# Optimization experiments

Hardware: AMD Instinct MI355X
Metric: run time of the kernel (lower is better)

Reference implementation:

```python
import jax, jax.numpy as jnp
import numpy as np

# ---- layer config (yolov3, layer_no=2) ----
STRIDE = 8
N_CLASSES = 80
IGNORE_TH = 0.7
ANCHORS_PX = np.array([[10,13],[16,30],[33,23],[30,61],[62,45],[59,119],[116,90],[156,198],[373,326]], np.float32)
ALL_ANCHORS = ANCHORS_PX / STRIDE          # [9,2] in grid units
ANCHOR_ID_LO, ANCHOR_ID_HI = 0, 2          # anchor_mask[2] = [0,1,2]
ANCHORS = ALL_ANCHORS[ANCHOR_ID_LO:ANCHOR_ID_HI+1]  # [3,2]
NA = 3
NC = N_CLASSES + 5

B, IN_CH, NG, NBOX = 16, 256, 76, 50


def _safe_log(p):
    # emulate torch BCE's log clamp at -100; eps stops 0*inf -> nan
    return jnp.maximum(jnp.log(jnp.maximum(p, 1e-12)), -100.0)


def _bce_sum(p, t, w=None):
    l = -(t * _safe_log(p) + (1.0 - t) * _safe_log(1.0 - p))
    if w is not None:
        l = l * w
    return l.sum()


def setup_inputs() -> dict:
    key = jax.random.key(0)
    k1, k2, k3, k4, k5 = jax.random.split(key, 5)
    xin = jax.random.normal(k1, (B, IN_CH, NG, NG), jnp.float32)
    cls = jax.random.randint(k2, (B, NBOX, 1), 0, N_CLASSES).astype(jnp.float32)
    cxy = jax.random.uniform(k3, (B, NBOX, 2), jnp.float32, 0.02, 0.98)
    wh = jax.random.uniform(k4, (B, NBOX, 2), jnp.float32, 0.02, 0.40)
    labels = jnp.concatenate([cls, cxy, wh], axis=-1)  # [B,N,5]
    W = jax.random.normal(k5, (NA * NC, IN_CH), jnp.float32) * 0.02  # 1x1 conv
    b = jnp.zeros((NA * NC,), jnp.float32)
    return {"xin": xin, "labels": labels, "W": W, "b": b}


def _yolo_loss(xin, labels, W, b):
    nB, _, nG, _ = xin.shape
    anchors = jnp.asarray(ANCHORS, xin.dtype)          # [3,2]
    all_anchors = jnp.asarray(ALL_ANCHORS, xin.dtype)  # [9,2]

    # 1x1 conv -> [B, A, G, G, C]
    x = jnp.einsum('bchw,oc->bohw', xin, W) + b[None, :, None, None]
    x = x.reshape(nB, NA, NC, nG, nG).transpose(0, 1, 3, 4, 2)

    xy = jax.nn.sigmoid(x[..., :2])
    wh = x[..., 2:4]
    conf_cls = jax.nn.sigmoid(x[..., 4:])  # [B,A,G,G,1+ncls]

    gy, gx = jnp.meshgrid(jnp.arange(nG, dtype=x.dtype), jnp.arange(nG, dtype=x.dtype), indexing='ij')
    pred_boxes = jnp.stack([
        xy[..., 0] + gx,
        xy[..., 1] + gy,
        jnp.exp(wh[..., 0]) * anchors[:, 0][None, :, None, None],
        jnp.exp(wh[..., 1]) * anchors[:, 1][None, :, None, None]], axis=-1)  # [B,A,G,G,4]

    # ---- ground truth ----
    valid = labels.sum(-1) > 0                     # [B,N]
    gt_cls = labels[..., 0].astype(jnp.int32)
    gt = labels[..., 1:] * nG                      # [B,N,4] cx,cy,w,h in grid units
    gt_x, gt_y, gt_w, gt_h = gt[..., 0], gt[..., 1], gt[..., 2], gt[..., 3]
    gi = jnp.floor(gt_x).astype(jnp.int32)
    gj = jnp.floor(gt_y).astype(jnp.int32)

    # best anchor per gt: wh-IoU vs all 9 anchors (centered at origin)
    inter_a = jnp.minimum(gt_w[..., None], all_anchors[:, 0]) * jnp.minimum(gt_h[..., None], all_anchors[:, 1])
    union_a = gt_w[..., None] * gt_h[..., None] + all_anchors[:, 0] * all_anchors[:, 1] - inter_a
    best = jnp.argmax(inter_a / union_a, axis=-1)  # [B,N]
    in_mask = (best >= ANCHOR_ID_LO) & (best <= ANCHOR_ID_HI)
    a = jnp.where(in_mask, best % 3, -1)           # [B,N]

    # all-pairs IoU: pred boxes vs gt boxes (ignore mask)
    pb = pred_boxes.reshape(nB, -1, 4)             # [B,M,4], M = A*G*G
    pa_area = pb[..., 2] * pb[..., 3]
    gt_area = gt_w * gt_h
    tl = jnp.maximum(pb[:, :, None, :2] - pb[:, :, None, 2:] / 2, gt[:, None, :, :2] - gt[:, None, :, 2:] / 2)
    br = jnp.minimum(pb[:, :, None, :2] + pb[:, :, None, 2:] / 2, gt[:, None, :, :2] + gt[:, None, :, 2:] / 2)
    inter = jnp.prod(br - tl, -1) * jnp.all(tl < br, -1)
    iou = inter / (pa_area[:, :, None] + gt_area[:, None, :] - inter)
    iou = jnp.where(valid[:, None, :], iou, 0.0)
    best_iou = iou.max(-1)                         # [B,M]
    has_boxes = valid.any(-1)
    obj_mask = jnp.where(has_boxes[:, None], best_iou <= IGNORE_TH, True).reshape(nB, NA, nG, nG)

    # ---- scatter target assignment ----
    assign = valid & (a >= 0)
    a_safe = jnp.clip(a, 0, NA - 1)
    aw = anchors[a_safe, 0]
    ah = anchors[a_safe, 1]
    tvec = jnp.concatenate([
        (gt_x - jnp.floor(gt_x))[..., None],
        (gt_y - jnp.floor(gt_y))[..., None],
        jnp.log(gt_w / aw + 1e-16)[..., None],
        jnp.log(gt_h / ah + 1e-16)[..., None],
        jnp.ones_like(gt_x)[..., None],
        jax.nn.one_hot(gt_cls, N_CLASSES, dtype=x.dtype)], axis=-1)  # [B,N,NC]
    sval = 2.0 - gt_w * gt_h / (nG * nG)

    bf = jnp.broadcast_to(jnp.arange(nB)[:, None], a.shape).reshape(-1)
    af = jnp.where(assign, a_safe, NA).reshape(-1)  # NA is OOB -> dropped
    jf = gj.reshape(-1)
    if_ = gi.reshape(-1)

    target = jnp.zeros((nB, NA, nG, nG, NC), x.dtype).at[bf, af, jf, if_].set(tvec.reshape(-1, NC), mode='drop')
    scale = jnp.zeros((nB, NA, nG, nG), x.dtype).at[bf, af, jf, if_].set(sval.reshape(-1), mode='drop')
    obj_mask = obj_mask.at[bf, af, jf, if_].set(True, mode='drop')
    noobj = jnp.zeros((nB, NA, nG, nG), bool).at[bf, af, jf, if_].set(True, mode='drop')

    # ---- losses ----
    nm = noobj.astype(x.dtype)[..., None]
    p_obj = conf_cls[..., 0] * obj_mask
    t_obj = target[..., 4] * obj_mask
    p_xy = xy * nm
    t_xy = target[..., :2] * nm
    p_wh = wh * nm
    t_wh = target[..., 2:4] * nm
    p_cls = conf_cls[..., 1:] * nm
    t_cls = target[..., 5:] * nm
    sc = scale[..., None]

    loss_xy = _bce_sum(p_xy, t_xy, sc)
    rs = jnp.sqrt(sc)
    loss_wh = 0.5 * jnp.sum((p_wh * rs - t_wh * rs) ** 2)
    loss_obj = _bce_sum(p_obj, t_obj)
    loss_cls = _bce_sum(p_cls, t_cls)
    loss = loss_xy + loss_wh + loss_obj + loss_cls
    return jnp.stack([loss, loss_xy, loss_wh, loss_obj, loss_cls])


def reference(xin, labels, W, b):
    return _yolo_loss(xin, labels, W, b)
```

## Files before the change

kernel.cpp:

```cpp
#include <hip/hip_runtime.h>
#include <math.h>

#define NB    16
#define NAg   3
#define NCg   85
#define NCLS  80
#define NGg   76
#define NSp   (NGg*NGg)
#define NBOX  50
#define INCH  256

#define ACC_OFF  0
#define HAS_OFF  32
#define WT_OFF   128
#define GB_OFF   (WT_OFF + 16384)
#define GA_OFF   (GB_OFF + 25600)
#define GI_OFF   (GA_OFF + 25600)
#define ZERO_BYTES 96

__device__ __constant__ float c_AW[9] = {1.25f,2.0f,4.125f,3.75f,7.75f,7.375f,14.5f,19.5f,46.625f};
__device__ __constant__ float c_AH[9] = {1.625f,3.75f,2.875f,7.625f,5.625f,14.875f,11.25f,24.75f,40.75f};

__device__ __forceinline__ float safe_log(float p) {
    return fmaxf(logf(fmaxf(p, 1e-12f)), -100.0f);
}
__device__ __forceinline__ float sigm(float x) {
    return 1.0f / (1.0f + expf(-x));
}

__global__ __launch_bounds__(256) void k_labels(
    const float* __restrict__ labels, const float* __restrict__ W,
    float* __restrict__ Wt, float* __restrict__ gbox, float* __restrict__ gaux,
    int* __restrict__ gint, int* __restrict__ hasAny)
{
    const int t = blockIdx.x * 256 + threadIdx.x;

    if (t < INCH * 16) {
        const int c = t >> 4, f = t & 15;
        Wt[t] = (f < 15) ? W[((f / 5) * NCg + (f % 5)) * INCH + c] : 0.f;
    }
    if (t >= NB * NBOX) return;
    const int b = t / NBOX;

    const float* L = labels + (size_t)t * 5;
    const float l0 = L[0], l1 = L[1], l2 = L[2], l3 = L[3], l4 = L[4];
    const int valid = (l0 + l1 + l2 + l3 + l4) > 0.f;

    const float gx = l1 * NGg, gy = l2 * NGg, gw = l3 * NGg, gh = l4 * NGg;

    int best = 0; float brr = -1.f;
#pragma unroll
    for (int k = 0; k < 9; k++) {
        float inter = fminf(gw, c_AW[k]) * fminf(gh, c_AH[k]);
        float uni   = gw*gh + c_AW[k]*c_AH[k] - inter;
        float r     = inter / uni;
        if (r > brr) { brr = r; best = k; }
    }
    const int a = (best <= 2) ? best : -1;
    const int assign = valid && (a >= 0);
    const int a_safe = a < 0 ? 0 : (a > 2 ? 2 : a);

    const int gi = (int)floorf(gx), gj = (int)floorf(gy);
    const int inb = (gi >= 0) && (gi < NGg) && (gj >= 0) && (gj < NGg);
    const int cell = (assign && inb) ? (a * NSp + gj * NGg + gi) : -1;

    float* gb = gbox + (size_t)t * 8;
    gb[0] = gx - gw * 0.5f;
    gb[1] = gy - gh * 0.5f;
    gb[2] = gx + gw * 0.5f;
    gb[3] = gy + gh * 0.5f;
    gb[4] = valid ? gw * gh : -1.f;
    gb[5] = __int_as_float(cell);

    float* ga = gaux + (size_t)t * 8;
    ga[0] = gx - floorf(gx);
    ga[1] = gy - floorf(gy);
    ga[2] = logf(gw / c_AW[a_safe] + 1e-16f);
    ga[3] = logf(gh / c_AH[a_safe] + 1e-16f);
    ga[4] = 2.f - gw * gh / (float)NSp;

    gint[t*2 + 0] = cell;
    gint[t*2 + 1] = (int)l0;

    if (valid) atomicOr(&hasAny[b], 1);
}

__global__ __launch_bounds__(64) void k_main(
    const float* __restrict__ xin, const float* __restrict__ Wt,
    const float* __restrict__ bias, const float* __restrict__ gbox,
    const int* __restrict__ hasAny, float* __restrict__ acc)
{
    const int b = blockIdx.y;
    const int s = blockIdx.x * 64 + threadIdx.x;

    float l = 0.f;
    if (s < NSp) {
        float accv[15];
#pragma unroll
        for (int f = 0; f < 15; ++f) accv[f] = 0.f;

        const float* xp = xin + (size_t)b * INCH * NSp + s;
#pragma unroll 2
        for (int c0 = 0; c0 < INCH; c0 += 8) {
            float v[8];
#pragma unroll
            for (int k = 0; k < 8; ++k) v[k] = xp[(size_t)(c0 + k) * NSp];
#pragma unroll
            for (int k = 0; k < 8; ++k) {
                const float* wr = Wt + ((c0 + k) << 4);
#pragma unroll
                for (int f = 0; f < 15; ++f) accv[f] += wr[f] * v[k];
            }
        }

        const int sy = s / NGg;
        const int sx = s - sy * NGg;
        const float gxf = (float)sx, gyf = (float)sy;

        float pbx0[3], pby0[3], pbx1[3], pby1[3], pa[3], cf[3];
#pragma unroll
        for (int a = 0; a < 3; ++a) {
            const float px = sigm(accv[a*5+0] + bias[a*NCg+0]) + gxf;
            const float py = sigm(accv[a*5+1] + bias[a*NCg+1]) + gyf;
            const float pw = expf(accv[a*5+2] + bias[a*NCg+2]) * c_AW[a];
            const float ph = expf(accv[a*5+3] + bias[a*NCg+3]) * c_AH[a];
            cf[a]  = sigm(accv[a*5+4] + bias[a*NCg+4]);
            pbx0[a] = px - pw * 0.5f;  pby0[a] = py - ph * 0.5f;
            pbx1[a] = px + pw * 0.5f;  pby1[a] = py + ph * 0.5f;
            pa[a]   = pw * ph;
        }

        bool ex0 = false, ex1 = false, ex2 = false;
        bool as0 = false, as1 = false, as2 = false;
        const float* gb = gbox + (size_t)b * NBOX * 8;
        for (int n = 0; n < NBOX; ++n) {
            const float bx0 = gb[n*8+0], by0 = gb[n*8+1];
            const float bx1 = gb[n*8+2], by1 = gb[n*8+3];
            const float gar = gb[n*8+4];
            const int cell  = __float_as_int(gb[n*8+5]);
            const int d = cell - s;
            as0 = as0 || (d == 0);
            as1 = as1 || (d == NSp);
            as2 = as2 || (d == 2*NSp);
            if (gar >= 0.f) {
#pragma unroll
                for (int a = 0; a < 3; ++a) {
                    const float tlx = fmaxf(pbx0[a], bx0);
                    const float tly = fmaxf(pby0[a], by0);
                    const float brx = fminf(pbx1[a], bx1);
                    const float bry = fminf(pby1[a], by1);
                    const float dx = brx - tlx, dy = bry - tly;
                    const float inter = (dx > 0.f && dy > 0.f) ? dx * dy : 0.f;
                    const bool hit = inter > 0.7f * (pa[a] + gar - inter);
                    if      (a == 0) ex0 = ex0 || hit;
                    else if (a == 1) ex1 = ex1 || hit;
                    else             ex2 = ex2 || hit;
                }
            }
        }

        const bool hasB = hasAny[b] != 0;
#pragma unroll
        for (int a = 0; a < 3; ++a) {
            const bool ex = (a == 0) ? ex0 : ((a == 1) ? ex1 : ex2);
            const bool as = (a == 0) ? as0 : ((a == 1) ? as1 : as2);
            const bool maskpre = hasB ? (!ex) : true;
            if (maskpre || as) {
                const float c = cf[a];
                l += as ? -safe_log(c) : -safe_log(1.f - c);
            }
        }
    }

#pragma unroll
    for (int off = 32; off > 0; off >>= 1) l += __shfl_down(l, off);
    if (threadIdx.x == 0) atomicAdd(&acc[2], l);
}

__global__ __launch_bounds__(256) void k_assigned(
    const float* __restrict__ xin, const float* __restrict__ W,
    const float* __restrict__ bias, const float* __restrict__ gaux,
    const int* __restrict__ gint, float* __restrict__ acc)
{
    const int t = blockIdx.x;
    const int b = t / NBOX, n = t % NBOX;
    const int cell = gint[t*2];
    if (cell < 0) return;
    for (int n2 = n + 1; n2 < NBOX; ++n2)
        if (gint[(b*NBOX + n2)*2] == cell) return;

    const int a = cell / NSp, s = cell % NSp;
    const int o0 = a * NCg;
    const int tid = threadIdx.x;

    __shared__ float4 col4[64];
    __shared__ float  xsh[NCg];
    __shared__ float  sacc[3];

    ((float*)col4)[tid] = xin[((size_t)b * INCH + tid) * NSp + s];
    if (tid < 3) sacc[tid] = 0.f;
    __syncthreads();

    const int wid = tid >> 6, lane = tid & 63;
    for (int o = wid; o < NCg; o += 4) {
        const float4 wv = *(const float4*)&W[(size_t)(o0 + o) * INCH + lane * 4];
        const float4 cv = col4[lane];
        float p = wv.x*cv.x + wv.y*cv.y + wv.z*cv.z + wv.w*cv.w;
        for (int off = 32; off; off >>= 1) p += __shfl_down(p, off);
        if (lane == 0) xsh[o] = p + bias[o0 + o];
    }
    __syncthreads();

    if (tid < NCg) {
        const float* ga = gaux + (size_t)t * 8;
        const float sval = ga[4];
        const int gcls = gint[t*2 + 1];
        float val = xsh[tid];
        float term; int slot;
        if (tid < 2) {
            float tgt = ga[tid];
            float p = sigm(val);
            term = -(tgt * safe_log(p) + (1.f - tgt) * safe_log(1.f - p)) * sval;
            slot = 0;
        } else if (tid < 4) {
            float tgt = ga[tid];
            float d = val - tgt;
            term = 0.5f * sval * d * d;
            slot = 1;
        } else if (tid == 4) {
            term = 0.f; slot = 2;
        } else {
            float tgt = ((tid - 5) == gcls) ? 1.f : 0.f;
            float p = sigm(val);
            term = -(tgt * safe_log(p) + (1.f - tgt) * safe_log(1.f - p));
            slot = 2;
        }
        atomicAdd(&sacc[slot], term);
    }
    __syncthreads();
    if (tid == 0) {
        atomicAdd(&acc[0], sacc[0]);
        atomicAdd(&acc[1], sacc[1]);
        atomicAdd(&acc[3], sacc[2]);
    }
}

__global__ void k_final(const float* __restrict__ acc, float* __restrict__ out)
{
    float xy = acc[0], wh = acc[1], ob = acc[2], cl = acc[3];
    out[0] = xy + wh + ob + cl;
    out[1] = xy; out[2] = wh; out[3] = ob; out[4] = cl;
}

extern "C" void kernel_launch(void* const* d_in, const int* in_sizes, int n_in,
                              void* d_out, int out_size, void* d_ws, size_t ws_size,
                              hipStream_t stream)
{
    const float* xin    = (const float*)d_in[0];
    const float* labels = (const float*)d_in[1];
    const float* W      = (const float*)d_in[2];
    const float* bias   = (const float*)d_in[3];

    char* ws = (char*)d_ws;
    float* acc    = (float*)(ws + ACC_OFF);
    int*   hasAny = (int*)  (ws + HAS_OFF);
    float* Wt     = (float*)(ws + WT_OFF);
    float* gbox   = (float*)(ws + GB_OFF);
    float* gaux   = (float*)(ws + GA_OFF);
    int*   gint   = (int*)  (ws + GI_OFF);
    float* out    = (float*)d_out;

    hipMemsetAsync(ws, 0, ZERO_BYTES, stream);

    k_labels<<<16, 256, 0, stream>>>(labels, W, Wt, gbox, gaux, gint, hasAny);

    k_main<<<dim3((NSp + 63) / 64, NB), 64, 0, stream>>>(xin, Wt, bias, gbox, hasAny, acc);

    k_assigned<<<dim3(NB * NBOX), 256, 0, stream>>>(xin, W, bias, gaux, gint, acc);

    k_final<<<1, 1, 0, stream>>>(acc, out);
}
```

Measured before the change: 236.1 us.

## Split channel reduction and box loop across four waves per block in main kernel

The main kernel moves from 64-thread blocks to 256-thread blocks. Each of the four waves reduces a quarter of the input channels for the same 64 spatial positions, and the partial sums are combined through shared memory. The ground-truth box IoU loop is also split across the waves, with the results merged through OR-ed bitmasks in shared memory. The memset is folded into the labels kernel, which now assigns one block per batch and computes hasAny with a ballot instead of atomics. This raises parallelism and memory-level concurrency on the bandwidth-bound 1x1 conv, at the cost of extra shared-memory traffic and barriers.

Result: no change. 231.7 us (-1.9%).

```diff
diff --git a/kernel.cpp b/kernel.cpp
--- a/kernel.cpp
+++ b/kernel.cpp
@@ -16,7 +16,6 @@
 #define GB_OFF   (WT_OFF + 16384)
 #define GA_OFF   (GB_OFF + 25600)
 #define GI_OFF   (GA_OFF + 25600)
-#define ZERO_BYTES 96
 
 __device__ __constant__ float c_AW[9] = {1.25f,2.0f,4.125f,3.75f,7.75f,7.375f,14.5f,19.5f,46.625f};
 __device__ __constant__ float c_AH[9] = {1.625f,3.75f,2.875f,7.625f,5.625f,14.875f,11.25f,24.75f,40.75f};
@@ -31,117 +30,146 @@
 __global__ __launch_bounds__(256) void k_labels(
     const float* __restrict__ labels, const float* __restrict__ W,
     float* __restrict__ Wt, float* __restrict__ gbox, float* __restrict__ gaux,
-    int* __restrict__ gint, int* __restrict__ hasAny)
-{
-    const int t = blockIdx.x * 256 + threadIdx.x;
-
-    if (t < INCH * 16) {
+    int* __restrict__ gint, int* __restrict__ hasAny, float* __restrict__ acc)
+{
+    const int b = blockIdx.x, tid = threadIdx.x;
+    const int t = b * 256 + tid;
+
+    {
         const int c = t >> 4, f = t & 15;
         Wt[t] = (f < 15) ? W[((f / 5) * NCg + (f % 5)) * INCH + c] : 0.f;
     }
-    if (t >= NB * NBOX) return;
-    const int b = t / NBOX;
-
-    const float* L = labels + (size_t)t * 5;
-    const float l0 = L[0], l1 = L[1], l2 = L[2], l3 = L[3], l4 = L[4];
-    const int valid = (l0 + l1 + l2 + l3 + l4) > 0.f;
-
-    const float gx = l1 * NGg, gy = l2 * NGg, gw = l3 * NGg, gh = l4 * NGg;
-
-    int best = 0; float brr = -1.f;
-#pragma unroll
-    for (int k = 0; k < 9; k++) {
-        float inter = fminf(gw, c_AW[k]) * fminf(gh, c_AH[k]);
-        float uni   = gw*gh + c_AW[k]*c_AH[k] - inter;
-        float r     = inter / uni;
-        if (r > brr) { brr = r; best = k; }
-    }
-    const int a = (best <= 2) ? best : -1;
-    const int assign = valid && (a >= 0);
-    const int a_safe = a < 0 ? 0 : (a > 2 ? 2 : a);
-
-    const int gi = (int)floorf(gx), gj = (int)floorf(gy);
-    const int inb = (gi >= 0) && (gi < NGg) && (gj >= 0) && (gj < NGg);
-    const int cell = (assign && inb) ? (a * NSp + gj * NGg + gi) : -1;
-
-    float* gb = gbox + (size_t)t * 8;
-    gb[0] = gx - gw * 0.5f;
-    gb[1] = gy - gh * 0.5f;
-    gb[2] = gx + gw * 0.5f;
-    gb[3] = gy + gh * 0.5f;
-    gb[4] = valid ? gw * gh : -1.f;
-    gb[5] = __int_as_float(cell);
-
-    float* ga = gaux + (size_t)t * 8;
-    ga[0] = gx - floorf(gx);
-    ga[1] = gy - floorf(gy);
-    ga[2] = logf(gw / c_AW[a_safe] + 1e-16f);
-    ga[3] = logf(gh / c_AH[a_safe] + 1e-16f);
-    ga[4] = 2.f - gw * gh / (float)NSp;
-
-    gint[t*2 + 0] = cell;
-    gint[t*2 + 1] = (int)l0;
-
-    if (valid) atomicOr(&hasAny[b], 1);
-}
-
-__global__ __launch_bounds__(64) void k_main(
+    if (b == 0 && tid < 8) acc[tid] = 0.f;
+
+    int valid = 0;
+    if (tid < NBOX) {
+        const int bt = b * NBOX + tid;
+        const float* L = labels + (size_t)bt * 5;
+        const float l0 = L[0], l1 = L[1], l2 = L[2], l3 = L[3], l4 = L[4];
+        valid = (l0 + l1 + l2 + l3 + l4) > 0.f;
+
+        const float gx = l1 * NGg, gy = l2 * NGg, gw = l3 * NGg, gh = l4 * NGg;
+
+        int best = 0; float brr = -1.f;
+#pragma unroll
+        for (int k = 0; k < 9; k++) {
+            float inter = fminf(gw, c_AW[k]) * fminf(gh, c_AH[k]);
+            float uni   = gw*gh + c_AW[k]*c_AH[k] - inter;
+            float r     = inter / uni;
+            if (r > brr) { brr = r; best = k; }
+        }
+        const int a = (best <= 2) ? best : -1;
+        const int assign = valid && (a >= 0);
+        const int a_safe = a < 0 ? 0 : (a > 2 ? 2 : a);
+
+        const int gi = (int)floorf(gx), gj = (int)floorf(gy);
+        const int inb = (gi >= 0) && (gi < NGg) && (gj >= 0) && (gj < NGg);
+        const int cell = (assign && inb) ? (a * NSp + gj * NGg + gi) : -1;
+
+        float* gb = gbox + (size_t)bt * 8;
+        gb[0] = gx - gw * 0.5f;
+        gb[1] = gy - gh * 0.5f;
+        gb[2] = gx + gw * 0.5f;
+        gb[3] = gy + gh * 0.5f;
+        gb[4] = valid ? gw * gh : -1.f;
+        gb[5] = __int_as_float(cell);
+
+        float* ga = gaux + (size_t)bt * 8;
+        ga[0] = gx - floorf(gx);
+        ga[1] = gy - floorf(gy);
+        ga[2] = logf(gw / c_AW[a_safe] + 1e-16f);
+        ga[3] = logf(gh / c_AH[a_safe] + 1e-16f);
+        ga[4] = 2.f - gw * gh / (float)NSp;
+
+        gint[bt*2 + 0] = cell;
+        gint[bt*2 + 1] = (int)l0;
+    }
+    if (tid < 64) {
+        const unsigned long long m = __ballot(valid != 0);
+        if (tid == 0) hasAny[b] = (m != 0ULL) ? 1 : 0;
+    }
+}
+
+__global__ __launch_bounds__(256) void k_main(
     const float* __restrict__ xin, const float* __restrict__ Wt,
     const float* __restrict__ bias, const float* __restrict__ gbox,
     const int* __restrict__ hasAny, float* __restrict__ acc)
 {
-    const int b = blockIdx.y;
-    const int s = blockIdx.x * 64 + threadIdx.x;
-
-    float l = 0.f;
-    if (s < NSp) {
-        float accv[15];
-#pragma unroll
-        for (int f = 0; f < 15; ++f) accv[f] = 0.f;
-
-        const float* xp = xin + (size_t)b * INCH * NSp + s;
+    __shared__ float partial[15 * 256];
+    __shared__ float red[15 * 64];
+    __shared__ int   smask[256];
+
+    const int b   = blockIdx.y;
+    const int tid = threadIdx.x;
+    const int w   = tid >> 6, l = tid & 63;
+    const int s   = blockIdx.x * 64 + l;
+    const bool live = (s < NSp);
+
+    float accv[15];
+#pragma unroll
+    for (int f = 0; f < 15; ++f) accv[f] = 0.f;
+
+    if (live) {
+        const float* xp = xin + ((size_t)b * INCH + w * 64) * NSp + s;
+        const float* wp = Wt + (w * 64) * 16;
 #pragma unroll 2
-        for (int c0 = 0; c0 < INCH; c0 += 8) {
+        for (int c0 = 0; c0 < 64; c0 += 8) {
             float v[8];
 #pragma unroll
             for (int k = 0; k < 8; ++k) v[k] = xp[(size_t)(c0 + k) * NSp];
 #pragma unroll
             for (int k = 0; k < 8; ++k) {
-                const float* wr = Wt + ((c0 + k) << 4);
+                const float* wr = wp + ((c0 + k) << 4);
 #pragma unroll
                 for (int f = 0; f < 15; ++f) accv[f] += wr[f] * v[k];
             }
         }
-
+    }
+#pragma unroll
+    for (int f = 0; f < 15; ++f) partial[f * 256 + tid] = accv[f];
+    __syncthreads();
+
+    for (int f = w; f < 15; f += 4) {
+        red[f * 64 + l] = partial[f * 256 + l]       + partial[f * 256 + 64 + l]
+                        + partial[f * 256 + 128 + l] + partial[f * 256 + 192 + l];
+    }
+    __syncthreads();
+
+    float cf[3];
+    int mask = 0;
+    if (live) {
         const int sy = s / NGg;
         const int sx = s - sy * NGg;
         const float gxf = (float)sx, gyf = (float)sy;
 
-        float pbx0[3], pby0[3], pbx1[3], pby1[3], pa[3], cf[3];
+        float pbx0[3], pby0[3], pbx1[3], pby1[3], pa[3];
 #pragma unroll
         for (int a = 0; a < 3; ++a) {
-            const float px = sigm(accv[a*5+0] + bias[a*NCg+0]) + gxf;
-            const float py = sigm(accv[a*5+1] + bias[a*NCg+1]) + gyf;
-            const float pw = expf(accv[a*5+2] + bias[a*NCg+2]) * c_AW[a];
-            const float ph = expf(accv[a*5+3] + bias[a*NCg+3]) * c_AH[a];
-            cf[a]  = sigm(accv[a*5+4] + bias[a*NCg+4]);
+            const float x0 = red[(a*5+0) * 64 + l];
+            const float x1 = red[(a*5+1) * 64 + l];
+            const float x2 = red[(a*5+2) * 64 + l];
+            const float x3 = red[(a*5+3) * 64 + l];
+            const float x4 = red[(a*5+4) * 64 + l];
+            const float px = sigm(x0 + bias[a*NCg+0]) + gxf;
+            const float py = sigm(x1 + bias[a*NCg+1]) + gyf;
+            const float pw = expf(x2 + bias[a*NCg+2]) * c_AW[a];
+            const float ph = expf(x3 + bias[a*NCg+3]) * c_AH[a];
+            cf[a]   = sigm(x4 + bias[a*NCg+4]);
             pbx0[a] = px - pw * 0.5f;  pby0[a] = py - ph * 0.5f;
             pbx1[a] = px + pw * 0.5f;  pby1[a] = py + ph * 0.5f;
             pa[a]   = pw * ph;
         }
 
-        bool ex0 = false, ex1 = false, ex2 = false;
-        bool as0 = false, as1 = false, as2 = false;
         const float* gb = gbox + (size_t)b * NBOX * 8;
-        for (int n = 0; n < NBOX; ++n) {
+        for (int n = w; n < NBOX; n += 4) {
             const float bx0 = gb[n*8+0], by0 = gb[n*8+1];
             const float bx1 = gb[n*8+2], by1 = gb[n*8+3];
             const float gar = gb[n*8+4];
             const int cell  = __float_as_int(gb[n*8+5]);
             const int d = cell - s;
-            as0 = as0 || (d == 0);
-            as1 = as1 || (d == NSp);
-            as2 = as2 || (d == 2*NSp);
+            if (d == 0)       mask |= 8;
+            if (d == NSp)     mask |= 16;
+            if (d == 2*NSp)   mask |= 32;
             if (gar >= 0.f) {
 #pragma unroll
                 for (int a = 0; a < 3; ++a) {
@@ -151,30 +179,34 @@
                     const float bry = fminf(pby1[a], by1);
                     const float dx = brx - tlx, dy = bry - tly;
                     const float inter = (dx > 0.f && dy > 0.f) ? dx * dy : 0.f;
-                    const bool hit = inter > 0.7f * (pa[a] + gar - inter);
-                    if      (a == 0) ex0 = ex0 || hit;
-                    else if (a == 1) ex1 = ex1 || hit;
-                    else             ex2 = ex2 || hit;
+                    if (inter > 0.7f * (pa[a] + gar - inter)) mask |= (1 << a);
                 }
             }
         }
-
-        const bool hasB = hasAny[b] != 0;
-#pragma unroll
-        for (int a = 0; a < 3; ++a) {
-            const bool ex = (a == 0) ? ex0 : ((a == 1) ? ex1 : ex2);
-            const bool as = (a == 0) ? as0 : ((a == 1) ? as1 : as2);
-            const bool maskpre = hasB ? (!ex) : true;
-            if (maskpre || as) {
-                const float c = cf[a];
-                l += as ? -safe_log(c) : -safe_log(1.f - c);
+    }
+    smask[tid] = mask;
+    __syncthreads();
+
+    if (w == 0) {
+        float lsum = 0.f;
+        if (live) {
+            const int m = smask[l] | smask[64 + l] | smask[128 + l] | smask[192 + l];
+            const bool hasB = hasAny[b] != 0;
+#pragma unroll
+            for (int a = 0; a < 3; ++a) {
+                const bool ex = (m & (1 << a)) != 0;
+                const bool as = (m & (8 << a)) != 0;
+                const bool maskpre = hasB ? (!ex) : true;
+                if (maskpre || as) {
+                    const float c = cf[a];
+                    lsum += as ? -safe_log(c) : -safe_log(1.f - c);
+                }
             }
         }
-    }
-
-#pragma unroll
-    for (int off = 32; off > 0; off >>= 1) l += __shfl_down(l, off);
-    if (threadIdx.x == 0) atomicAdd(&acc[2], l);
+#pragma unroll
+        for (int off = 32; off > 0; off >>= 1) lsum += __shfl_down(lsum, off);
+        if (l == 0) atomicAdd(&acc[2], lsum);
+    }
 }
 
 __global__ __launch_bounds__(256) void k_assigned(
@@ -184,18 +216,23 @@
 {
     const int t = blockIdx.x;
     const int b = t / NBOX, n = t % NBOX;
-    const int cell = gint[t*2];
-    if (cell < 0) return;
-    for (int n2 = n + 1; n2 < NBOX; ++n2)
-        if (gint[(b*NBOX + n2)*2] == cell) return;
-
-    const int a = cell / NSp, s = cell % NSp;
-    const int o0 = a * NCg;
     const int tid = threadIdx.x;
 
+    __shared__ int   scell[NBOX];
     __shared__ float4 col4[64];
     __shared__ float  xsh[NCg];
     __shared__ float  sacc[3];
+
+    if (tid < NBOX) scell[tid] = gint[(b * NBOX + tid) * 2];
+    __syncthreads();
+
+    const int cell = scell[n];
+    if (cell < 0) return;
+    for (int n2 = n + 1; n2 < NBOX; ++n2)
+        if (scell[n2] == cell) return;
+
+    const int a = cell / NSp, s = cell % NSp;
+    const int o0 = a * NCg;
 
     ((float*)col4)[tid] = xin[((size_t)b * INCH + tid) * NSp + s];
     if (tid < 3) sacc[tid] = 0.f;
@@ -270,11 +307,9 @@
     int*   gint   = (int*)  (ws + GI_OFF);
     float* out    = (float*)d_out;
 
-    hipMemsetAsync(ws, 0, ZERO_BYTES, stream);
-
-    k_labels<<<16, 256, 0, stream>>>(labels, W, Wt, gbox, gaux, gint, hasAny);
-
-    k_main<<<dim3((NSp + 63) / 64, NB), 64, 0, stream>>>(xin, Wt, bias, gbox, hasAny, acc);
+    k_labels<<<16, 256, 0, stream>>>(labels, W, Wt, gbox, gaux, gint, hasAny, acc);
+
+    k_main<<<dim3((NSp + 63) / 64, NB), 256, 0, stream>>>(xin, Wt, bias, gbox, hasAny, acc);
 
     k_assigned<<<dim3(NB * NBOX), 256, 0, stream>>>(xin, W, bias, gaux, gint, acc);
 
```
